# Performance work log

Measured on AMD Instinct MI355X. Metric: run time of the kernel, lower is better.

Reference implementation:

```python
import jax, jax.numpy as jnp
import numpy as np

B, N, H, W = 128, 8192, 7, 7


def setup_inputs() -> dict:
    key = jax.random.key(0)
    ks = jax.random.split(key, 10)
    inp = {
        'x': jax.random.normal(ks[0], (B, N, H, W), dtype=jnp.float32),
        'y': jax.random.normal(ks[1], (B, N), dtype=jnp.float32),
        # nn.MultiheadAttention(embed_dim=1, num_heads=1) params (all scalar)
        'wq': jax.random.normal(ks[2], (), dtype=jnp.float32),
        'wk': jax.random.normal(ks[3], (), dtype=jnp.float32),
        'wv': jax.random.normal(ks[4], (), dtype=jnp.float32),
        'bq': jax.random.normal(ks[5], (), dtype=jnp.float32) * 0.1,
        'bk': jax.random.normal(ks[6], (), dtype=jnp.float32) * 0.1,
        'bv': jax.random.normal(ks[7], (), dtype=jnp.float32) * 0.1,
        'wo': jax.random.normal(ks[8], (), dtype=jnp.float32),
        'bo': jax.random.normal(ks[9], (), dtype=jnp.float32) * 0.1,
    }
    return inp


def _mha1(q_src, kv_src, wq, bq, wk, bk, wv, bv, wo, bo):
    # embed_dim=1, num_heads=1, scale = 1/sqrt(1) = 1.
    # torch sees (seq=B, batch=N, embed=1): attention mixes the B axis per n.
    q = q_src * wq + bq            # [B, N]
    k = kv_src * wk + bk           # [B, N]
    v = kv_src * wv + bv           # [B, N]
    scores = jnp.einsum('in,jn->ijn', q, k)      # [B, B, N]
    a = jax.nn.softmax(scores, axis=1)           # softmax over keys j
    out = jnp.einsum('ijn,jn->in', a, v)         # [B, N]
    return out * wo + bo


def reference(x, y, wq, bq, wk, bk, wv, bv, wo, bo):
    xp = jnp.mean(x, axis=(2, 3))                # AdaptiveAvgPool2d((1,1)) -> [B, N]
    self_x = _mha1(xp, xp, wq, bq, wk, bk, wv, bv, wo, bo)
    self_y = _mha1(y, y, wq, bq, wk, bk, wv, bv, wo, bo)
    cross_x = _mha1(xp, y, wq, bq, wk, bk, wv, bv, wo, bo)
    cross_y = _mha1(y, xp, wq, bq, wk, bk, wv, bv, wo, bo)
    f_x = xp + self_x
    f_y = y + self_y
    c_f_x = cross_x + f_x
    c_f_y = cross_y + f_y
    return jnp.concatenate((c_f_x, c_f_y), axis=1)   # [B, 2N]
```

## Files before the change

kernel.cpp:

```cpp
#include <hip/hip_runtime.h>


constexpr int B_SEQ = 128;
constexpr int N_COL = 8192;
constexpr int HWP   = 49;
constexpr int NT    = 256;
constexpr int TC    = 4;

__global__ __launch_bounds__(NT, 4) void rsca_fused(
    const float* __restrict__ x, const float* __restrict__ y,
    const float* __restrict__ pwq, const float* __restrict__ pwk,
    const float* __restrict__ pwv, const float* __restrict__ pbq,
    const float* __restrict__ pbk, const float* __restrict__ pbv,
    const float* __restrict__ pwo, const float* __restrict__ pbo,
    float* __restrict__ out)
{
    __shared__ float2 kvxT[TC][B_SEQ];
    __shared__ float2 kvyT[TC][B_SEQ];
    __shared__ float  pmn[2][TC][8], pmx[2][TC][8];
    __shared__ float  klmn[2][TC], klmx[2][TC];

    const int t  = threadIdx.x;
    const int n0 = blockIdx.x * TC;

    const float wq = pwq[0], wk = pwk[0], wv = pwv[0];
    const float bq = pbq[0], bk = pbk[0], bv = pbv[0];
    const float wo = pwo[0], bo = pbo[0];
    const float L2E = 1.4426950408889634f;
    const float wkL = wk * L2E, bkL = bk * L2E;
    const float alpha = wo * wv;
    const float beta2 = 2.0f * (wo * bv + bo);

    for (int cell = t; cell < B_SEQ * TC; cell += NT) {
        const int j = cell >> 2, c = cell & 3;
        const float fy = y[(size_t)j * N_COL + n0 + c];
        kvyT[c][j] = make_float2(fmaf(fy, wkL, bkL), fy);
    }

    const int ql  = t & 3;
    const int seg = t >> 2;
    for (int pass = 0; pass < 2; ++pass) {
        const int j = pass * 64 + seg;
        const float4* __restrict__ base =
            (const float4*)(x + ((size_t)j * N_COL + n0) * (size_t)HWP);
        float s0 = 0.f, s1 = 0.f, s2 = 0.f, s3 = 0.f;
        float4 v;
        v = base[ql +  0]; s0 += v.x + v.y + v.z + v.w;
        v = base[ql +  4]; s0 += v.x + v.y + v.z + v.w;
        v = base[ql +  8]; s0 += v.x + v.y + v.z + v.w;
        v = base[ql + 16]; s1 += v.x + v.y + v.z + v.w;
        v = base[ql + 20]; s1 += v.x + v.y + v.z + v.w;
        v = base[ql + 28]; s2 += v.x + v.y + v.z + v.w;
        v = base[ql + 32]; s2 += v.x + v.y + v.z + v.w;
        v = base[ql + 40]; s3 += v.x + v.y + v.z + v.w;
        v = base[ql + 44]; s3 += v.x + v.y + v.z + v.w;
        v = base[ql + 12];
        { const float sm = v.x + v.y + v.z + v.w;
          const float cr = (ql == 0) ? v.x : 0.0f;
          s0 += cr; s1 += sm - cr; }
        v = base[ql + 24];
        { const float sm = v.x + v.y + v.z + v.w;
          const float cr = (ql == 0) ? (v.x + v.y) : 0.0f;
          s1 += cr; s2 += sm - cr; }
        v = base[ql + 36];
        { const float sm = v.x + v.y + v.z + v.w;
          const float cr = (ql == 0) ? (v.x + v.y + v.z) : 0.0f;
          s2 += cr; s3 += sm - cr; }
        v = base[48];
        const float tail = v.x + v.y + v.z + v.w;
        s0 += __shfl_xor(s0, 1); s1 += __shfl_xor(s1, 1);
        s2 += __shfl_xor(s2, 1); s3 += __shfl_xor(s3, 1);
        s0 += __shfl_xor(s0, 2); s1 += __shfl_xor(s1, 2);
        s2 += __shfl_xor(s2, 2); s3 += __shfl_xor(s3, 2);
        float r = s0;
        r = (ql == 1) ? s1 : r;
        r = (ql == 2) ? s2 : r;
        r = (ql == 3) ? (s3 + tail) : r;
        const float mean = r * (1.0f / HWP);
        kvxT[ql][j] = make_float2(fmaf(mean, wkL, bkL), mean);
    }
    __syncthreads();

    if (t < 64) {
        const int set = t >> 5, c = (t >> 3) & 3, part = t & 7;
        float mn = 3.4e38f, mx = -3.4e38f;
        #pragma unroll
        for (int k = 0; k < 16; ++k) {
            const int j = part * 16 + k;
            const float vv = set ? kvyT[c][j].x : kvxT[c][j].x;
            mn = fminf(mn, vv);
            mx = fmaxf(mx, vv);
        }
        pmn[set][c][part] = mn;
        pmx[set][c][part] = mx;
    }
    __syncthreads();
    if (t < 8) {
        const int set = t >> 2, c = t & 3;
        float mn = 3.4e38f, mx = -3.4e38f;
        #pragma unroll
        for (int k = 0; k < 8; ++k) {
            mn = fminf(mn, pmn[set][c][k]);
            mx = fmaxf(mx, pmx[set][c][k]);
        }
        klmn[set][c] = mn;
        klmx[set][c] = mx;
    }
    __syncthreads();

    const int i  = t & (B_SEQ - 1);
    const int ch = t >> 7;
    #pragma unroll
    for (int cc = 0; cc < 2; ++cc) {
        const int c = ch * 2 + cc;
        const float2* __restrict__ px = kvxT[c];
        const float2* __restrict__ py = kvyT[c];
        const float xi = px[i].y;
        const float yi = py[i].y;
        const float qx = fmaf(xi, wq, bq);
        const float qy = fmaf(yi, wq, bq);
        const float nmsx = -(qx >= 0.0f ? qx * klmx[0][c] : qx * klmn[0][c]);
        const float nmcy = -(qy >= 0.0f ? qy * klmx[0][c] : qy * klmn[0][c]);
        const float nmsy = -(qy >= 0.0f ? qy * klmx[1][c] : qy * klmn[1][c]);
        const float nmcx = -(qx >= 0.0f ? qx * klmx[1][c] : qx * klmn[1][c]);

        float s0sx = 0.f, s1sx = 0.f, s0cy = 0.f, s1cy = 0.f;
        float s0sy = 0.f, s1sy = 0.f, s0cx = 0.f, s1cx = 0.f;
        for (int j0 = 0; j0 < B_SEQ; j0 += 8) {
            float2 kx[8], ky[8];
            #pragma unroll
            for (int jj = 0; jj < 8; ++jj) kx[jj] = px[j0 + jj];
            #pragma unroll
            for (int jj = 0; jj < 8; ++jj) ky[jj] = py[j0 + jj];
            #pragma unroll
            for (int jj = 0; jj < 8; ++jj) {
                const float e1 = __builtin_amdgcn_exp2f(fmaf(qx, kx[jj].x, nmsx));
                const float e2 = __builtin_amdgcn_exp2f(fmaf(qy, kx[jj].x, nmcy));
                const float e3 = __builtin_amdgcn_exp2f(fmaf(qy, ky[jj].x, nmsy));
                const float e4 = __builtin_amdgcn_exp2f(fmaf(qx, ky[jj].x, nmcx));
                s1sx = fmaf(e1, kx[jj].y, s1sx); s0sx += e1;
                s1cy = fmaf(e2, kx[jj].y, s1cy); s0cy += e2;
                s1sy = fmaf(e3, ky[jj].y, s1sy); s0sy += e3;
                s1cx = fmaf(e4, ky[jj].y, s1cx); s0cx += e4;
            }
        }
        const float mx_attn = s1sx * __builtin_amdgcn_rcpf(s0sx)
                            + s1cx * __builtin_amdgcn_rcpf(s0cx);
        const float my_attn = s1sy * __builtin_amdgcn_rcpf(s0sy)
                            + s1cy * __builtin_amdgcn_rcpf(s0cy);
        out[(size_t)i * (2 * N_COL) + n0 + c]         = fmaf(alpha, mx_attn, beta2 + xi);
        out[(size_t)i * (2 * N_COL) + N_COL + n0 + c] = fmaf(alpha, my_attn, beta2 + yi);
    }
}

extern "C" void kernel_launch(void* const* d_in, const int* in_sizes, int n_in,
                              void* d_out, int out_size, void* d_ws, size_t ws_size,
                              hipStream_t stream) {
    const float* x   = (const float*)d_in[0];
    const float* y   = (const float*)d_in[1];
    const float* pwq = (const float*)d_in[2];
    const float* pwk = (const float*)d_in[3];
    const float* pwv = (const float*)d_in[4];
    const float* pbq = (const float*)d_in[5];
    const float* pbk = (const float*)d_in[6];
    const float* pbv = (const float*)d_in[7];
    const float* pwo = (const float*)d_in[8];
    const float* pbo = (const float*)d_in[9];
    float* out = (float*)d_out;

    rsca_fused<<<dim3(N_COL / TC), dim3(NT), 0, stream>>>(
        x, y, pwq, pwk, pwv, pbq, pbk, pbv, pwo, pbo, out);
}
```

Baseline: 333.1 us.

## Use packed FP32 FMA/add in attention loop, batch x loads, raise occupancy

The inner attention loop now uses v_pk_fma_f32 and v_pk_add_f32 through inline asm, which halves the number of FMA/add instructions per key around the exp2 calls. Each key is stored in shared memory as a duplicated float4 so the packed operands load directly. The x pooling loads are all issued before any reduction to raise memory-level parallelism, and launch bounds ask for 5 blocks per CU. The trade-offs are double the LDS footprint and traffic for the keys, more registers held by the 13 float4 loads, and inline asm that can block compiler scheduling.

```diff
diff --git a/kernel.cpp b/kernel.cpp
--- a/kernel.cpp
+++ b/kernel.cpp
@@ -7,7 +7,20 @@
 constexpr int NT    = 256;
 constexpr int TC    = 4;
 
-__global__ __launch_bounds__(NT, 4) void rsca_fused(
+typedef float v2f __attribute__((ext_vector_type(2)));
+
+static __device__ __forceinline__ v2f pk_fma(v2f a, v2f b, v2f c) {
+    v2f d;
+    asm("v_pk_fma_f32 %0, %1, %2, %3" : "=v"(d) : "v"(a), "v"(b), "v"(c));
+    return d;
+}
+static __device__ __forceinline__ v2f pk_add(v2f a, v2f b) {
+    v2f d;
+    asm("v_pk_add_f32 %0, %1, %2" : "=v"(d) : "v"(a), "v"(b));
+    return d;
+}
+
+__global__ __launch_bounds__(NT, 5) void rsca_fused(
     const float* __restrict__ x, const float* __restrict__ y,
     const float* __restrict__ pwq, const float* __restrict__ pwk,
     const float* __restrict__ pwv, const float* __restrict__ pbq,
@@ -15,8 +28,8 @@
     const float* __restrict__ pwo, const float* __restrict__ pbo,
     float* __restrict__ out)
 {
-    __shared__ float2 kvxT[TC][B_SEQ];
-    __shared__ float2 kvyT[TC][B_SEQ];
+    __shared__ float4 kvxT[TC][B_SEQ];
+    __shared__ float4 kvyT[TC][B_SEQ];
     __shared__ float  pmn[2][TC][8], pmx[2][TC][8];
     __shared__ float  klmn[2][TC], klmx[2][TC];
 
@@ -34,7 +47,8 @@
     for (int cell = t; cell < B_SEQ * TC; cell += NT) {
         const int j = cell >> 2, c = cell & 3;
         const float fy = y[(size_t)j * N_COL + n0 + c];
-        kvyT[c][j] = make_float2(fmaf(fy, wkL, bkL), fy);
+        const float kl = fmaf(fy, wkL, bkL);
+        kvyT[c][j] = make_float4(kl, kl, fy, fy);
     }
 
     const int ql  = t & 3;
@@ -43,31 +57,32 @@
         const int j = pass * 64 + seg;
         const float4* __restrict__ base =
             (const float4*)(x + ((size_t)j * N_COL + n0) * (size_t)HWP);
+        float4 v[13];
+        #pragma unroll
+        for (int k = 0; k < 12; ++k) v[k] = base[ql + 4 * k];
+        v[12] = base[48];
+
         float s0 = 0.f, s1 = 0.f, s2 = 0.f, s3 = 0.f;
-        float4 v;
-        v = base[ql +  0]; s0 += v.x + v.y + v.z + v.w;
-        v = base[ql +  4]; s0 += v.x + v.y + v.z + v.w;
-        v = base[ql +  8]; s0 += v.x + v.y + v.z + v.w;
-        v = base[ql + 16]; s1 += v.x + v.y + v.z + v.w;
-        v = base[ql + 20]; s1 += v.x + v.y + v.z + v.w;
-        v = base[ql + 28]; s2 += v.x + v.y + v.z + v.w;
-        v = base[ql + 32]; s2 += v.x + v.y + v.z + v.w;
-        v = base[ql + 40]; s3 += v.x + v.y + v.z + v.w;
-        v = base[ql + 44]; s3 += v.x + v.y + v.z + v.w;
-        v = base[ql + 12];
-        { const float sm = v.x + v.y + v.z + v.w;
-          const float cr = (ql == 0) ? v.x : 0.0f;
+        s0 += v[0].x + v[0].y + v[0].z + v[0].w;
+        s0 += v[1].x + v[1].y + v[1].z + v[1].w;
+        s0 += v[2].x + v[2].y + v[2].z + v[2].w;
+        s1 += v[4].x + v[4].y + v[4].z + v[4].w;
+        s1 += v[5].x + v[5].y + v[5].z + v[5].w;
+        s2 += v[7].x + v[7].y + v[7].z + v[7].w;
+        s2 += v[8].x + v[8].y + v[8].z + v[8].w;
+        s3 += v[10].x + v[10].y + v[10].z + v[10].w;
+        s3 += v[11].x + v[11].y + v[11].z + v[11].w;
+        { const float sm = v[3].x + v[3].y + v[3].z + v[3].w;
+          const float cr = (ql == 0) ? v[3].x : 0.0f;
           s0 += cr; s1 += sm - cr; }
-        v = base[ql + 24];
-        { const float sm = v.x + v.y + v.z + v.w;
-          const float cr = (ql == 0) ? (v.x + v.y) : 0.0f;
+        { const float sm = v[6].x + v[6].y + v[6].z + v[6].w;
+          const float cr = (ql == 0) ? (v[6].x + v[6].y) : 0.0f;
           s1 += cr; s2 += sm - cr; }
-        v = base[ql + 36];
-        { const float sm = v.x + v.y + v.z + v.w;
-          const float cr = (ql == 0) ? (v.x + v.y + v.z) : 0.0f;
+        { const float sm = v[9].x + v[9].y + v[9].z + v[9].w;
+          const float cr = (ql == 0) ? (v[9].x + v[9].y + v[9].z) : 0.0f;
           s2 += cr; s3 += sm - cr; }
-        v = base[48];
-        const float tail = v.x + v.y + v.z + v.w;
+        const float tail = v[12].x + v[12].y + v[12].z + v[12].w;
+
         s0 += __shfl_xor(s0, 1); s1 += __shfl_xor(s1, 1);
         s2 += __shfl_xor(s2, 1); s3 += __shfl_xor(s3, 1);
         s0 += __shfl_xor(s0, 2); s1 += __shfl_xor(s1, 2);
@@ -77,7 +92,8 @@
         r = (ql == 2) ? s2 : r;
         r = (ql == 3) ? (s3 + tail) : r;
         const float mean = r * (1.0f / HWP);
-        kvxT[ql][j] = make_float2(fmaf(mean, wkL, bkL), mean);
+        const float kl = fmaf(mean, wkL, bkL);
+        kvxT[ql][j] = make_float4(kl, kl, mean, mean);
     }
     __syncthreads();
 
@@ -113,10 +129,10 @@
     #pragma unroll
     for (int cc = 0; cc < 2; ++cc) {
         const int c = ch * 2 + cc;
-        const float2* __restrict__ px = kvxT[c];
-        const float2* __restrict__ py = kvyT[c];
-        const float xi = px[i].y;
-        const float yi = py[i].y;
+        const float4* __restrict__ px = kvxT[c];
+        const float4* __restrict__ py = kvyT[c];
+        const float xi = px[i].z;
+        const float yi = py[i].z;
         const float qx = fmaf(xi, wq, bq);
         const float qy = fmaf(yi, wq, bq);
         const float nmsx = -(qx >= 0.0f ? qx * klmx[0][c] : qx * klmn[0][c]);
@@ -124,30 +140,42 @@
         const float nmsy = -(qy >= 0.0f ? qy * klmx[1][c] : qy * klmn[1][c]);
         const float nmcx = -(qx >= 0.0f ? qx * klmx[1][c] : qx * klmn[1][c]);
 
-        float s0sx = 0.f, s1sx = 0.f, s0cy = 0.f, s1cy = 0.f;
-        float s0sy = 0.f, s1sy = 0.f, s0cx = 0.f, s1cx = 0.f;
-        for (int j0 = 0; j0 < B_SEQ; j0 += 8) {
-            float2 kx[8], ky[8];
+        const v2f q12  = { qx, qy };
+        const v2f q34  = { qy, qx };
+        const v2f nm12 = { nmsx, nmcy };
+        const v2f nm34 = { nmsy, nmcx };
+        v2f s0_12 = {0.f, 0.f}, s0_34 = {0.f, 0.f};
+        v2f s1_12 = {0.f, 0.f}, s1_34 = {0.f, 0.f};
+
+        for (int j0 = 0; j0 < B_SEQ; j0 += 4) {
+            float4 kx4[4], ky4[4];
             #pragma unroll
-            for (int jj = 0; jj < 8; ++jj) kx[jj] = px[j0 + jj];
+            for (int jj = 0; jj < 4; ++jj) kx4[jj] = px[j0 + jj];
             #pragma unroll
-            for (int jj = 0; jj < 8; ++jj) ky[jj] = py[j0 + jj];
+            for (int jj = 0; jj < 4; ++jj) ky4[jj] = py[j0 + jj];
             #pragma unroll
-            for (int jj = 0; jj < 8; ++jj) {
-                const float e1 = __builtin_amdgcn_exp2f(fmaf(qx, kx[jj].x, nmsx));
-                const float e2 = __builtin_amdgcn_exp2f(fmaf(qy, kx[jj].x, nmcy));
-                const float e3 = __builtin_amdgcn_exp2f(fmaf(qy, ky[jj].x, nmsy));
-                const float e4 = __builtin_amdgcn_exp2f(fmaf(qx, ky[jj].x, nmcx));
-                s1sx = fmaf(e1, kx[jj].y, s1sx); s0sx += e1;
-                s1cy = fmaf(e2, kx[jj].y, s1cy); s0cy += e2;
-                s1sy = fmaf(e3, ky[jj].y, s1sy); s0sy += e3;
-                s1cx = fmaf(e4, ky[jj].y, s1cx); s0cx += e4;
+            for (int jj = 0; jj < 4; ++jj) {
+                const v2f klx = { kx4[jj].x, kx4[jj].y };
+                const v2f rwx = { kx4[jj].z, kx4[jj].w };
+                const v2f kly = { ky4[jj].x, ky4[jj].y };
+                const v2f rwy = { ky4[jj].z, ky4[jj].w };
+                const v2f a12 = pk_fma(q12, klx, nm12);
+                const v2f a34 = pk_fma(q34, kly, nm34);
+                v2f e12, e34;
+                e12.x = __builtin_amdgcn_exp2f(a12.x);
+                e12.y = __builtin_amdgcn_exp2f(a12.y);
+                e34.x = __builtin_amdgcn_exp2f(a34.x);
+                e34.y = __builtin_amdgcn_exp2f(a34.y);
+                s1_12 = pk_fma(e12, rwx, s1_12);
+                s1_34 = pk_fma(e34, rwy, s1_34);
+                s0_12 = pk_add(s0_12, e12);
+                s0_34 = pk_add(s0_34, e34);
             }
         }
-        const float mx_attn = s1sx * __builtin_amdgcn_rcpf(s0sx)
-                            + s1cx * __builtin_amdgcn_rcpf(s0cx);
-        const float my_attn = s1sy * __builtin_amdgcn_rcpf(s0sy)
-                            + s1cy * __builtin_amdgcn_rcpf(s0cy);
+        const float mx_attn = s1_12.x * __builtin_amdgcn_rcpf(s0_12.x)
+                            + s1_34.y * __builtin_amdgcn_rcpf(s0_34.y);
+        const float my_attn = s1_34.x * __builtin_amdgcn_rcpf(s0_34.x)
+                            + s1_12.y * __builtin_amdgcn_rcpf(s0_12.y);
         out[(size_t)i * (2 * N_COL) + n0 + c]         = fmaf(alpha, mx_attn, beta2 + xi);
         out[(size_t)i * (2 * N_COL) + N_COL + n0 + c] = fmaf(alpha, my_attn, beta2 + yi);
     }
```

Result: no change. 335.2 us (+0.6%).
